# Optimization experiments

Measured on AMD Instinct MI355X. Metric: run time of the kernel, lower is better.

The kernel has to match this reference:

```python
import jax, jax.numpy as jnp
import numpy as np

K = 32        # max neighbors per query point
RADIUS = 0.1  # ball radius
N1 = 8192
N2 = 8192


def setup_inputs() -> dict:
    key = jax.random.key(0)
    k1, k2 = jax.random.split(key)
    points1 = jax.random.uniform(k1, (1, N1, 3), dtype=jnp.float32)
    points2 = jax.random.uniform(k2, (1, N2, 3), dtype=jnp.float32)
    lengths1 = jnp.full((1,), N1, dtype=jnp.int32)  # unused by the kernel, kept for API parity
    lengths2 = jnp.full((1,), N2, dtype=jnp.int32)
    return {"points1": points1, "points2": points2, "lengths1": lengths1, "lengths2": lengths2}


def _ball_query(p1, p2, k, radius):
    # p1: [N1,3], p2: [N2,3]
    # squared distances via gram trick, no [N1,N2,3] diff tensor
    d2 = (jnp.sum(p1 * p1, axis=-1)[:, None]
          + jnp.sum(p2 * p2, axis=-1)[None, :]
          - 2.0 * (p1 @ p2.T))                                   # [N1,N2]
    within = d2 <= radius * radius                                # kernel skips only if dist > radius
    n2 = p2.shape[0]
    # pick the first k in-range neighbors in index order (deterministic stand-in
    # for the unspecified hash-grid traversal order)
    score = jnp.where(within, jnp.arange(n2, dtype=jnp.int32), n2)  # [N1,N2]
    _, idx = jax.lax.top_k(-score, k)                             # k smallest scores -> first k indices
    valid = jnp.take_along_axis(within, idx, axis=1)              # [N1,k]
    counts = jnp.minimum(jnp.sum(within, axis=-1), k).astype(jnp.int32)  # [N1]
    mapping = jnp.where(valid, idx, 0).astype(jnp.int32)          # zeros-padded like the torch buffer
    outputs = jnp.where(valid[..., None], p2[mapping], 0.0)       # [N1,k,3]
    return mapping, counts, outputs


def reference(points1, points2, lengths1, lengths2):
    mapping, num_neighbors, outputs = _ball_query(points1[0], points2[0], K, RADIUS)
    return mapping[None], num_neighbors[None], outputs[None]
```

## Files before the change

### kernel.cpp

```cpp
#include <hip/hip_runtime.h>

#define N1 8192
#define N2 8192
#define KNN 32
#define R2_F32 0.009999999776482582f

#define GDIM 10
#define NCELLS (GDIM * GDIM * GDIM)
#define CELL_W 0.109375f
#define INV_W  9.142857142857142f
#define CAP 40
#define HCAP 128
#define PRUNE2 0.0105f

#define WS_CNT 0
#define WS_PTS 4096

struct F3 { float x, y, z; };

__device__ __forceinline__ F3 ld3(const float* __restrict__ p, int j) {
    F3 r;
    r.x = p[3 * j + 0];
    r.y = p[3 * j + 1];
    r.z = p[3 * j + 2];
    return r;
}

__device__ __forceinline__ int cell_coord(float v) {
    int c = (int)(v * INV_W);
    return c > (GDIM - 1) ? (GDIM - 1) : c;
}

__device__ __forceinline__ int prefix_lt(unsigned long long m) {
    return (int)__builtin_amdgcn_mbcnt_hi(
        (unsigned)(m >> 32),
        __builtin_amdgcn_mbcnt_lo((unsigned)m, 0u));
}

__global__ __launch_bounds__(256) void k_build(const float* __restrict__ p2,
                                               int* __restrict__ cnt,
                                               float4* __restrict__ pts) {
    __shared__ float4 buf[4][CAP];
    __shared__ int    cl[4];
    const int w    = (int)(threadIdx.x >> 6);
    const int lane = (int)(threadIdx.x & 63);
    const int c    = (int)blockIdx.x;
    const int ccx = c / 100, ccy = (c / 10) % 10, ccz = c % 10;

    int count = 0;
    const int jofs = w * (N2 / 4);

    auto proc = [&](const F3& p, int jb) {
        const bool match = (cell_coord(p.x) == ccx) &&
                           (cell_coord(p.y) == ccy) &&
                           (cell_coord(p.z) == ccz);
        const unsigned long long m = __ballot(match);
        if (m) {
            const int pos = count + prefix_lt(m);
            if (match && pos < CAP)
                buf[w][pos] = make_float4(p.x, p.y, p.z, (float)(jb + lane));
            count += (int)__popcll(m);
        }
    };

    constexpr int NMB = (N2 / 4) / 256;
    F3 b0 = ld3(p2, jofs + 0 * 64 + lane);
    F3 b1 = ld3(p2, jofs + 1 * 64 + lane);
    F3 b2 = ld3(p2, jofs + 2 * 64 + lane);
    F3 b3 = ld3(p2, jofs + 3 * 64 + lane);
    for (int mb = 0; mb < NMB; ++mb) {
        const int nb = (mb + 1 < NMB) ? (mb + 1) : 0;
        F3 n0 = ld3(p2, jofs + nb * 256 + 0 * 64 + lane);
        F3 n1 = ld3(p2, jofs + nb * 256 + 1 * 64 + lane);
        F3 n2 = ld3(p2, jofs + nb * 256 + 2 * 64 + lane);
        F3 n3 = ld3(p2, jofs + nb * 256 + 3 * 64 + lane);
        const int jb = jofs + mb * 256;
        proc(b0, jb + 0 * 64);
        proc(b1, jb + 1 * 64);
        proc(b2, jb + 2 * 64);
        proc(b3, jb + 3 * 64);
        b0 = n0; b1 = n1; b2 = n2; b3 = n3;
    }

    if (lane == 0) cl[w] = count;
    __syncthreads();

    const int c0 = cl[0], c1 = cl[1], c2 = cl[2], c3 = cl[3];
    int start = 0;
    if (w > 0) start += c0;
    if (w > 1) start += c1;
    if (w > 2) start += c2;
    const int st = start < CAP ? start : CAP;
    int ns = CAP - st;
    if (count < ns) ns = count;
    if (lane < ns) pts[c * CAP + st + lane] = buf[w][lane];
    if (w == 0 && lane == 0) cnt[c] = c0 + c1 + c2 + c3;
}

__global__ __launch_bounds__(256) void k_query(
    const float* __restrict__ p1, const float4* __restrict__ pts,
    const int* __restrict__ cnt,
    float* __restrict__ map_f, float* __restrict__ cnt_f, float* __restrict__ out_f)
{
    __shared__ float4 hits[4][HCAP];
    const int w    = (int)(threadIdx.x >> 6);
    const int lane = (int)(threadIdx.x & 63);
    const int q    = (int)blockIdx.x * 4 + w;

    const float qx = p1[3 * q], qy = p1[3 * q + 1], qz = p1[3 * q + 2];
    const float s1 = __fadd_rn(__fadd_rn(__fmul_rn(qx, qx), __fmul_rn(qy, qy)),
                               __fmul_rn(qz, qz));

    const int cx = cell_coord(qx), cy = cell_coord(qy), cz = cell_coord(qz);

    int len = 0, id = 0;
    if (lane < 27) {
        const int ax = cx + lane / 9 - 1;
        const int ay = cy + (lane / 3) % 3 - 1;
        const int az = cz + lane % 3 - 1;
        const bool valid = (unsigned)ax < GDIM && (unsigned)ay < GDIM && (unsigned)az < GDIM;
        if (valid) {
            id = (ax * GDIM + ay) * GDIM + az;
            const float gx = fmaxf(0.0f, fmaxf((float)ax * CELL_W - qx, qx - (float)(ax + 1) * CELL_W));
            const float gy = fmaxf(0.0f, fmaxf((float)ay * CELL_W - qy, qy - (float)(ay + 1) * CELL_W));
            const float gz = fmaxf(0.0f, fmaxf((float)az * CELL_W - qz, qz - (float)(az + 1) * CELL_W));
            const float mind2 = gx * gx + gy * gy + gz * gz;
            if (mind2 <= PRUNE2) {
                int c = cnt[id];
                len = c < CAP ? c : CAP;
            }
        }
    }

    int cum = len;
#pragma unroll
    for (int d = 1; d < 32; d <<= 1) {
        const int v = __shfl_up(cum, d, 64);
        if (lane >= d) cum += v;
    }
    const int T = __shfl(cum, 26, 64);
    const int adj = id * CAP - (cum - len);

    int hcnt = 0;
    for (int g0 = 0; g0 < T; g0 += 64) {
        const int g = g0 + lane;
        const bool active = g < T;
        int lo = 0;
#pragma unroll
        for (int st = 16; st > 0; st >>= 1) {
            const int v = __shfl(cum, lo + st - 1, 64);
            if (v <= g) lo += st;
        }
        const int aj = __shfl(adj, lo, 64);
        float4 e = make_float4(2.0f, 2.0f, 2.0f, 0.0f);
        if (active) e = pts[g + aj];
        const float s2  = __fadd_rn(__fadd_rn(__fmul_rn(e.x, e.x), __fmul_rn(e.y, e.y)),
                                    __fmul_rn(e.z, e.z));
        const float dot = __fmaf_rn(qz, e.z, __fmaf_rn(qy, e.y, __fmul_rn(qx, e.x)));
        const float d2  = __fsub_rn(__fadd_rn(s1, s2), __fadd_rn(dot, dot));
        const bool within = active && (d2 <= R2_F32);
        const unsigned long long m = __ballot(within);
        if (m) {
            const int pos = hcnt + prefix_lt(m);
            if (within && pos < HCAP) hits[w][pos] = e;
            hcnt += (int)__popcll(m);
        }
    }

    const int cap2 = hcnt < HCAP ? hcnt : HCAP;
    float4 e0, e1;
    int j0 = 0x7FFFFFFF, j1 = 0x7FFFFFFF;
    if (lane < cap2)      { e0 = hits[w][lane];      j0 = (int)e0.w; }
    if (lane + 64 < cap2) { e1 = hits[w][lane + 64]; j1 = (int)e1.w; }
    int r0 = 0, r1 = 0;
#pragma unroll 4
    for (int i = 0; i < cap2; ++i) {
        const int ji = (int)hits[w][i].w;
        r0 += (ji < j0) ? 1 : 0;
        r1 += (ji < j1) ? 1 : 0;
    }

    const int outc = hcnt < KNN ? hcnt : KNN;
    if (lane < cap2 && r0 < KNN) {
        const int s = q * KNN + r0;
        map_f[s] = e0.w;
        float* o = out_f + s * 3;
        o[0] = e0.x; o[1] = e0.y; o[2] = e0.z;
    }
    if (lane + 64 < cap2 && r1 < KNN) {
        const int s = q * KNN + r1;
        map_f[s] = e1.w;
        float* o = out_f + s * 3;
        o[0] = e1.x; o[1] = e1.y; o[2] = e1.z;
    }
    if (lane < KNN && lane >= outc) {
        const int s = q * KNN + lane;
        map_f[s] = 0.0f;
        float* o = out_f + s * 3;
        o[0] = 0.0f; o[1] = 0.0f; o[2] = 0.0f;
    }
    if (lane == 0) cnt_f[q] = (float)outc;
}

extern "C" void kernel_launch(void* const* d_in, const int* in_sizes, int n_in,
                              void* d_out, int out_size, void* d_ws, size_t ws_size,
                              hipStream_t stream) {
    const float* p1 = (const float*)d_in[0];
    const float* p2 = (const float*)d_in[1];
    float* out = (float*)d_out;

    float* map_f = out;
    float* cnt_f = out + (size_t)N1 * KNN;
    float* out_f = cnt_f + N1;

    char* ws = (char*)d_ws;
    int*    cnt = (int*)(ws + WS_CNT);
    float4* pts = (float4*)(ws + WS_PTS);

    hipLaunchKernelGGL(k_build, dim3(NCELLS), dim3(256), 0, stream, p2, cnt, pts);
    hipLaunchKernelGGL(k_query, dim3(N1 / 4), dim3(256), 0, stream,
                       p1, pts, cnt, map_f, cnt_f, out_f);
}
```

Baseline: 21.23 us.

## Build four grid cells per block with eight waves scanning points

The grid-build kernel now handles four consecutive cells per block and uses eight waves of 512 threads, each scanning 1/8 of points2. Each point's cell id is computed once and ballot-compacted against four target cells. This cuts the redundant full scans of points2 across 1000 blocks down to 250 blocks. The cost is four ballots per point and more shared memory per block.

```diff
diff --git a/kernel.cpp b/kernel.cpp
--- a/kernel.cpp
+++ b/kernel.cpp
@@ -16,6 +16,10 @@
 #define WS_CNT 0
 #define WS_PTS 4096
 
+#define BW  8
+#define BSL (N2 / BW)
+#define CPB 4
+
 struct F3 { float x, y, z; };
 
 __device__ __forceinline__ F3 ld3(const float* __restrict__ p, int j) {
@@ -37,33 +41,35 @@
         __builtin_amdgcn_mbcnt_lo((unsigned)m, 0u));
 }
 
-__global__ __launch_bounds__(256) void k_build(const float* __restrict__ p2,
+__global__ __launch_bounds__(512) void k_build(const float* __restrict__ p2,
                                                int* __restrict__ cnt,
                                                float4* __restrict__ pts) {
-    __shared__ float4 buf[4][CAP];
-    __shared__ int    cl[4];
+    __shared__ float4 buf[BW][CPB][CAP];
+    __shared__ int    cl[BW][CPB];
     const int w    = (int)(threadIdx.x >> 6);
     const int lane = (int)(threadIdx.x & 63);
-    const int c    = (int)blockIdx.x;
-    const int ccx = c / 100, ccy = (c / 10) % 10, ccz = c % 10;
-
-    int count = 0;
-    const int jofs = w * (N2 / 4);
+    const int base = (int)blockIdx.x * CPB;
+
+    int count[CPB] = {0, 0, 0, 0};
+    const int jofs = w * BSL;
 
     auto proc = [&](const F3& p, int jb) {
-        const bool match = (cell_coord(p.x) == ccx) &&
-                           (cell_coord(p.y) == ccy) &&
-                           (cell_coord(p.z) == ccz);
-        const unsigned long long m = __ballot(match);
-        if (m) {
-            const int pos = count + prefix_lt(m);
-            if (match && pos < CAP)
-                buf[w][pos] = make_float4(p.x, p.y, p.z, (float)(jb + lane));
-            count += (int)__popcll(m);
+        const int cid = (cell_coord(p.x) * GDIM + cell_coord(p.y)) * GDIM + cell_coord(p.z);
+        const unsigned dt = (unsigned)(cid - base);
+#pragma unroll
+        for (int t = 0; t < CPB; ++t) {
+            const bool match = (dt == (unsigned)t);
+            const unsigned long long m = __ballot(match);
+            if (m) {
+                const int pos = count[t] + prefix_lt(m);
+                if (match && pos < CAP)
+                    buf[w][t][pos] = make_float4(p.x, p.y, p.z, (float)(jb + lane));
+                count[t] += (int)__popcll(m);
+            }
         }
     };
 
-    constexpr int NMB = (N2 / 4) / 256;
+    constexpr int NMB = BSL / 256;
     F3 b0 = ld3(p2, jofs + 0 * 64 + lane);
     F3 b1 = ld3(p2, jofs + 1 * 64 + lane);
     F3 b2 = ld3(p2, jofs + 2 * 64 + lane);
@@ -82,19 +88,29 @@
         b0 = n0; b1 = n1; b2 = n2; b3 = n3;
     }
 
-    if (lane == 0) cl[w] = count;
+    if (lane == 0) {
+        cl[w][0] = count[0];
+        cl[w][1] = count[1];
+        cl[w][2] = count[2];
+        cl[w][3] = count[3];
+    }
     __syncthreads();
 
-    const int c0 = cl[0], c1 = cl[1], c2 = cl[2], c3 = cl[3];
-    int start = 0;
-    if (w > 0) start += c0;
-    if (w > 1) start += c1;
-    if (w > 2) start += c2;
-    const int st = start < CAP ? start : CAP;
-    int ns = CAP - st;
-    if (count < ns) ns = count;
-    if (lane < ns) pts[c * CAP + st + lane] = buf[w][lane];
-    if (w == 0 && lane == 0) cnt[c] = c0 + c1 + c2 + c3;
+#pragma unroll
+    for (int t = 0; t < CPB; ++t) {
+        int startv = 0, tot = 0;
+#pragma unroll
+        for (int u = 0; u < BW; ++u) {
+            const int cu = cl[u][t];
+            if (u < w) startv += cu;
+            tot += cu;
+        }
+        const int st = startv < CAP ? startv : CAP;
+        int ns = CAP - st;
+        if (count[t] < ns) ns = count[t];
+        if (lane < ns) pts[(base + t) * CAP + st + lane] = buf[w][t][lane];
+        if (w == 0 && lane == 0) cnt[base + t] = tot;
+    }
 }
 
 __global__ __launch_bounds__(256) void k_query(
@@ -217,7 +233,7 @@
     int*    cnt = (int*)(ws + WS_CNT);
     float4* pts = (float4*)(ws + WS_PTS);
 
-    hipLaunchKernelGGL(k_build, dim3(NCELLS), dim3(256), 0, stream, p2, cnt, pts);
-    hipLaunchKernelGGL(k_query, dim3(N1 / 4), dim3(256), 0, stream,
+    hipLaunchKernelGGL(k_build, dim3(NCELLS / CPB), dim3(512), 0, stream, p2, cnt, pts);
+    hipLaunchKernelGGL(k_query, dim3(N1 / 4),       dim3(256), 0, stream,
                        p1, pts, cnt, map_f, cnt_f, out_f);
 }
```

Result: faster. 19.43 us (-8.5%).
